# Kernel optimization log

Measured on AMD Instinct MI355X. Metric: run time of the kernel, lower is better.

Reference implementation:

```python
import jax, jax.numpy as jnp
import numpy as np

B, N, DIM, H, DH = 4, 2048, 1024, 16, 64
ROT = 32               # rotary dim (half of head dim)
INNER = H * DH         # 1024


def rotate_every_two(x):
    # (... (d j)) with j=2: pairs (x1, x2) -> (-x2, x1), interleaved back
    x1 = x[..., ::2]
    x2 = x[..., 1::2]
    return jnp.stack((-x2, x1), axis=-1).reshape(x.shape)


def setup_inputs() -> dict:
    key = jax.random.key(0)
    k1, k2, k3 = jax.random.split(key, 3)
    x = jax.random.normal(k1, (B, N, DIM), dtype=jnp.float32)
    # standard rotary sin/cos tables, [N, ROT], pairs share a frequency
    pos = jnp.arange(N, dtype=jnp.float32)[:, None]
    inv_freq = 1.0 / (10000.0 ** (jnp.arange(0, ROT, 2, dtype=jnp.float32) / ROT))
    ang = jnp.repeat(pos * inv_freq, 2, axis=-1)  # [N, ROT]
    sin, cos = jnp.sin(ang), jnp.cos(ang)
    Wqkv = jax.random.normal(k2, (DIM, 3 * INNER), dtype=jnp.float32) * (DIM ** -0.5)
    Wout = jax.random.normal(k3, (INNER, DIM), dtype=jnp.float32) * (INNER ** -0.5)
    return {"x": x, "sin": sin, "cos": cos, "Wqkv": Wqkv, "Wout": Wout}


def reference(x, sin, cos, Wqkv, Wout):
    scale = DH ** -0.5
    qkv = x @ Wqkv                                  # [B, N, 3*INNER]
    q, k, v = jnp.split(qkv, 3, axis=-1)

    def split_heads(t):  # 'b n (h d) -> (b h) n d'
        return t.reshape(B, N, H, DH).transpose(0, 2, 1, 3).reshape(B * H, N, DH)

    q, k, v = map(split_heads, (q, k, v))
    q = q * scale                                   # scale before RoPE (as in source)

    rd = sin.shape[-1]

    def rope(t):
        t_rot, t_pass = t[..., :rd], t[..., rd:]
        t_rot = t_rot * cos + rotate_every_two(t_rot) * sin
        return jnp.concatenate((t_rot, t_pass), axis=-1)

    q, k = rope(q), rope(k)

    sim = jnp.einsum('bid,bjd->bij', q, k)          # [(B*H), N, N]
    attn_w = jax.nn.softmax(sim, axis=-1)
    out = jnp.einsum('bij,bjd->bid', attn_w, v)     # [(B*H), N, DH]

    out = out.reshape(B, H, N, DH).transpose(0, 2, 1, 3).reshape(B, N, INNER)
    return out @ Wout                               # [B, N, DIM]
```

## Files before the change

kernel.cpp:

```cpp
#include <hip/hip_runtime.h>

typedef unsigned short u16;
typedef __attribute__((ext_vector_type(8))) short short8;
typedef __attribute__((ext_vector_type(4))) float f32x4;

#define DEV __device__ __forceinline__

DEV u16 f2bf(float f) {
  unsigned u = __float_as_uint(f);
  u += 0x7FFF + ((u >> 16) & 1);
  return (u16)(u >> 16);
}
DEV float bf2f(u16 b) { return __uint_as_float(((unsigned)b) << 16); }

DEV unsigned pk_trunc(float a, float b) {
  return __builtin_amdgcn_perm(__float_as_uint(b), __float_as_uint(a), 0x07060302u);
}

DEV void g2l16(const u16* g, u16* l) {
  __builtin_amdgcn_global_load_lds((__attribute__((address_space(1))) void*)(g),
                                   (__attribute__((address_space(3))) void*)(l), 16, 0, 0);
}

__global__ __launch_bounds__(256) void k_prep(const float* __restrict__ x,
                                              u16* __restrict__ xb,
                                              const float* __restrict__ Wqkv,
                                              u16* __restrict__ wqkvT,
                                              const float* __restrict__ Wout,
                                              u16* __restrict__ woutT) {
  __shared__ float t[32][33];
  const int blk = blockIdx.x;
  if (blk < 8192) {
    int i = blk * 256 + threadIdx.x;
    float4 v = ((const float4*)x)[i];
    ushort4 r;
    r.x = f2bf(v.x); r.y = f2bf(v.y); r.z = f2bf(v.z); r.w = f2bf(v.w);
    ((ushort4*)xb)[i] = r;
    return;
  }
  const float* W;
  u16* Wt;
  int K = 1024, N, local;
  if (blk < 11264) {
    W = Wqkv; Wt = wqkvT; N = 3072; local = blk - 8192;
  } else {
    W = Wout; Wt = woutT; N = 1024; local = blk - 11264;
  }
  int nb = N / 32;
  int n0 = (local % nb) * 32, k0 = (local / nb) * 32;
  int tx = threadIdx.x & 31, ty = threadIdx.x >> 5;
#pragma unroll
  for (int i = 0; i < 4; ++i)
    t[ty + i * 8][tx] = W[(size_t)(k0 + ty + i * 8) * N + n0 + tx];
  __syncthreads();
#pragma unroll
  for (int i = 0; i < 4; ++i)
    Wt[(size_t)(n0 + ty + i * 8) * K + k0 + tx] = f2bf(t[tx][ty + i * 8]);
}

template <int EPI>
__global__ __launch_bounds__(256) void k_gemm(
    const u16* __restrict__ A, const u16* __restrict__ Bt,
    int M, int N, int K,
    u16* __restrict__ qw, u16* __restrict__ kw, u16* __restrict__ vw,
    float* __restrict__ of, const float* __restrict__ sn,
    const float* __restrict__ cs, float qscale) {
  __shared__ __align__(16) u16 As[128 * 64];
  __shared__ __align__(16) u16 Bs[128 * 64];
  const int t = threadIdx.x;
  const int wv = t >> 6, lane = t & 63;
  const int a15 = lane & 15, g = lane >> 4;
  const int wr = wv >> 1, wc = wv & 1;
  int m0, n0;
  if (EPI == 0) {
    int id = blockIdx.x;
    int c = id & 7, j = id >> 3;
    m0 = (j & 63) * 128;
    n0 = (c * 3 + (j >> 6)) * 128;
  } else {
    m0 = blockIdx.x * 128;
    n0 = blockIdx.y * 128;
  }
  const int gr = lane >> 3, gc = (lane & 7) * 8;

  f32x4 acc[4][4];
#pragma unroll
  for (int i = 0; i < 4; ++i)
#pragma unroll
    for (int j = 0; j < 4; ++j)
#pragma unroll
      for (int r = 0; r < 4; ++r) acc[i][j][r] = 0.f;

  for (int k0 = 0; k0 < K; k0 += 64) {
#pragma unroll
    for (int c4 = 0; c4 < 4; ++c4) {
      int c = wv * 4 + c4;
      g2l16(A + (size_t)(m0 + c * 8 + gr) * K + k0 + gc, &As[c * 512]);
      g2l16(Bt + (size_t)(n0 + c * 8 + gr) * K + k0 + gc, &Bs[c * 512]);
    }
    __syncthreads();
#pragma unroll
    for (int ks = 0; ks < 2; ++ks) {
      short8 af[4], bf[4];
#pragma unroll
      for (int mi = 0; mi < 4; ++mi)
        af[mi] = *(const short8*)&As[(wr * 64 + mi * 16 + a15) * 64 + ks * 32 + g * 8];
#pragma unroll
      for (int ni = 0; ni < 4; ++ni)
        bf[ni] = *(const short8*)&Bs[(wc * 64 + ni * 16 + a15) * 64 + ks * 32 + g * 8];
#pragma unroll
      for (int mi = 0; mi < 4; ++mi)
#pragma unroll
        for (int ni = 0; ni < 4; ++ni)
          acc[mi][ni] = __builtin_amdgcn_mfma_f32_16x16x32_bf16(af[mi], bf[ni], acc[mi][ni], 0, 0, 0);
    }
    __syncthreads();
  }

  if (EPI == 0) {
    const int part = n0 >> 10;
    if (part <= 1) {
      const float sc = (part == 0) ? qscale : 1.f;
      u16* dst = (part == 0) ? qw : kw;
#pragma unroll
      for (int mi = 0; mi < 4; ++mi) {
#pragma unroll
        for (int ni = 0; ni < 4; ++ni) {
          int col = n0 + wc * 64 + ni * 16 + a15;
          int rem = col & 1023, h = rem >> 6, d = rem & 63;
          int row = m0 + wr * 64 + mi * 16 + g * 4;
          int b = row >> 11, n = row & 2047;
          size_t bh = (size_t)b * 16 + h;
#pragma unroll
          for (int r = 0; r < 4; ++r) {
            float v = acc[mi][ni][r];
            float p = __shfl_xor(v, 1);
            float outv = v;
            if (d < 32) {
              int nr = n + r;
              float c = cs[nr * 32 + d], s = sn[nr * 32 + d];
              outv = v * c + ((d & 1) ? p * s : -p * s);
            }
            dst[(bh * 2048 + n + r) * 64 + d] = f2bf(outv * sc);
          }
        }
      }
    } else {
#pragma unroll
      for (int mi = 0; mi < 4; ++mi) {
#pragma unroll
        for (int ni = 0; ni < 4; ++ni) {
          int col = n0 + wc * 64 + ni * 16 + a15;
          int rem = col & 1023, h = rem >> 6, d = rem & 63;
          int row = m0 + wr * 64 + mi * 16 + g * 4;
          int b = row >> 11, n = row & 2047;
          size_t bh = (size_t)b * 16 + h;
          ushort4 pk;
          pk.x = f2bf(acc[mi][ni][0]); pk.y = f2bf(acc[mi][ni][1]);
          pk.z = f2bf(acc[mi][ni][2]); pk.w = f2bf(acc[mi][ni][3]);
          *(ushort4*)&vw[(bh * 64 + d) * 2048 + n] = pk;
        }
      }
    }
  } else {
#pragma unroll
    for (int mi = 0; mi < 4; ++mi)
#pragma unroll
      for (int ni = 0; ni < 4; ++ni) {
        int col = n0 + wc * 64 + ni * 16 + a15;
        int row = m0 + wr * 64 + mi * 16 + g * 4;
#pragma unroll
        for (int r = 0; r < 4; ++r)
          of[(size_t)(row + r) * N + col] = acc[mi][ni][r];
      }
  }
}

__global__ __launch_bounds__(256, 3) void k_attn(
    const u16* __restrict__ q, const u16* __restrict__ kk, const u16* __restrict__ vT,
    u16* __restrict__ o) {
  __shared__ __align__(16) u16 Ks[2][4096];
  __shared__ __align__(16) u16 Vs[2][4096];
  __shared__ __align__(16) u16 Pl[4][1024];
  const int t = threadIdx.x;
  const int w = t >> 6, lane = t & 63;
  const int a15 = lane & 15, g = lane >> 4;
  const int id = blockIdx.x;
  const int bh = (id & 7) | ((id >> 7) << 3);
  const int qb = (id >> 3) & 15;
  const int q0 = qb * 128 + w * 32;
  const size_t hb = (size_t)bh * (2048 * 64);

  short8 qf[2][2];
#pragma unroll
  for (int f = 0; f < 2; ++f)
#pragma unroll
    for (int h = 0; h < 2; ++h)
      qf[f][h] = *(const short8*)&q[hb + (size_t)(q0 + f * 16 + a15) * 64 + h * 32 + g * 8];

  int ksrc[2], vsrc[2];
#pragma unroll
  for (int c = 0; c < 2; ++c) {
    int L = w * 2048 + c * 1024 + lane * 16;
    int row = L >> 7;
    int sb = L ^ ((row & 7) << 4);
    ksrc[c] = sb >> 1;
    vsrc[c] = row * 2048 + ((sb & 127) >> 1);
  }
  const u16* kg = kk + hb;
  const u16* vg = vT + (size_t)bh * (64 * 2048);

#define STAGE(b, j0) do {                                        \
    g2l16(kg + (size_t)(j0) * 64 + ksrc[0], &Ks[b][w * 1024]);   \
    g2l16(kg + (size_t)(j0) * 64 + ksrc[1], &Ks[b][w * 1024 + 512]); \
    g2l16(vg + (j0) + vsrc[0], &Vs[b][w * 1024]);                \
    g2l16(vg + (j0) + vsrc[1], &Vs[b][w * 1024 + 512]);          \
  } while (0)

  const f32x4 z4 = {0.f, 0.f, 0.f, 0.f};
  const short8 ones = {(short)0x3F80, (short)0x3F80, (short)0x3F80, (short)0x3F80,
                       (short)0x3F80, (short)0x3F80, (short)0x3F80, (short)0x3F80};
  f32x4 accO[2][4], ssum[2];
#pragma unroll
  for (int f = 0; f < 2; ++f) {
    ssum[f] = z4;
#pragma unroll
    for (int dc = 0; dc < 4; ++dc) accO[f][dc] = z4;
  }

  STAGE(0, 0);
  int cur = 0;
  for (int jt = 0; jt < 32; ++jt) {
    __syncthreads();
    if (jt < 31) STAGE(cur ^ 1, (jt + 1) * 64);

    f32x4 st[2][4];
    const char* Kb = (const char*)Ks[cur];
    __builtin_amdgcn_s_setprio(1);
#pragma unroll
    for (int jc = 0; jc < 4; ++jc) {
      int row = jc * 16 + a15;
      int sw = (row & 7) << 4;
      short8 ka0 = *(const short8*)(Kb + ((row * 128 + g * 16) ^ sw));
      short8 ka1 = *(const short8*)(Kb + ((row * 128 + 64 + g * 16) ^ sw));
      st[0][jc] = __builtin_amdgcn_mfma_f32_16x16x32_bf16(ka0, qf[0][0], z4, 0, 0, 0);
      st[0][jc] = __builtin_amdgcn_mfma_f32_16x16x32_bf16(ka1, qf[0][1], st[0][jc], 0, 0, 0);
      st[1][jc] = __builtin_amdgcn_mfma_f32_16x16x32_bf16(ka0, qf[1][0], z4, 0, 0, 0);
      st[1][jc] = __builtin_amdgcn_mfma_f32_16x16x32_bf16(ka1, qf[1][1], st[1][jc], 0, 0, 0);
    }
    __builtin_amdgcn_s_setprio(0);
    short8 vf[2][4];
    const char* Vb = (const char*)Vs[cur];
#pragma unroll
    for (int kt = 0; kt < 2; ++kt)
#pragma unroll
      for (int dc = 0; dc < 4; ++dc) {
        int row = dc * 16 + a15;
        vf[kt][dc] = *(const short8*)(Vb + ((row * 128 + kt * 64 + g * 16) ^ ((row & 7) << 4)));
      }
#pragma unroll
    for (int f = 0; f < 2; ++f) {
#pragma unroll
      for (int jc = 0; jc < 4; ++jc) {
        float e0 = __builtin_amdgcn_exp2f(st[f][jc][0]);
        float e1 = __builtin_amdgcn_exp2f(st[f][jc][1]);
        float e2 = __builtin_amdgcn_exp2f(st[f][jc][2]);
        float e3 = __builtin_amdgcn_exp2f(st[f][jc][3]);
        uint2 pw;
        pw.x = pk_trunc(e0, e1);
        pw.y = pk_trunc(e2, e3);
        int byte = (a15 * 128 + (jc * 16 + g * 4) * 2) ^ ((a15 & 7) << 4);
        *(uint2*)((char*)Pl[w] + byte) = pw;
      }
      __builtin_amdgcn_s_setprio(1);
#pragma unroll
      for (int kt = 0; kt < 2; ++kt) {
        int byteA = (a15 * 128 + kt * 64 + g * 16) ^ ((a15 & 7) << 4);
        short8 pa = *(const short8*)((const char*)Pl[w] + byteA);
        ssum[f] = __builtin_amdgcn_mfma_f32_16x16x32_bf16(pa, ones, ssum[f], 0, 0, 0);
#pragma unroll
        for (int dc = 0; dc < 4; ++dc)
          accO[f][dc] = __builtin_amdgcn_mfma_f32_16x16x32_bf16(pa, vf[kt][dc], accO[f][dc], 0, 0, 0);
      }
      __builtin_amdgcn_s_setprio(0);
    }
    cur ^= 1;
  }
#undef STAGE

  const int b = bh >> 4, h = bh & 15;
#pragma unroll
  for (int f = 0; f < 2; ++f) {
    float rs[4];
#pragma unroll
    for (int r = 0; r < 4; ++r) rs[r] = 1.f / ssum[f][r];
#pragma unroll
    for (int dc = 0; dc < 4; ++dc)
#pragma unroll
      for (int r = 0; r < 4; ++r) {
        int n = q0 + f * 16 + g * 4 + r;
        o[((size_t)b * 2048 + n) * 1024 + h * 64 + dc * 16 + a15] = f2bf(accO[f][dc][r] * rs[r]);
      }
  }
}

extern "C" void kernel_launch(void* const* d_in, const int* in_sizes, int n_in,
                              void* d_out, int out_size, void* d_ws, size_t ws_size,
                              hipStream_t stream) {
  const float* x = (const float*)d_in[0];
  const float* sn = (const float*)d_in[1];
  const float* cs = (const float*)d_in[2];
  const float* Wqkv = (const float*)d_in[3];
  const float* Wout = (const float*)d_in[4];
  float* out = (float*)d_out;

  u16* ws = (u16*)d_ws;
  u16* xb = ws;
  u16* wqkvT = xb + 8192ull * 1024;
  u16* woutT = wqkvT + 3072ull * 1024;
  u16* qw = woutT + 1024ull * 1024;
  u16* kw = qw + 64ull * 2048 * 64;
  u16* vw = kw + 64ull * 2048 * 64;
  u16* attn = xb;

  const float qscale = 0.125f * 1.4426950408889634f;

  k_prep<<<12288, 256, 0, stream>>>(x, xb, Wqkv, wqkvT, Wout, woutT);
  k_gemm<0><<<1536, 256, 0, stream>>>(xb, wqkvT, 8192, 3072, 1024,
                                      qw, kw, vw, nullptr, sn, cs, qscale);
  k_attn<<<1024, 256, 0, stream>>>(qw, kw, vw, attn);
  k_gemm<1><<<dim3(64, 8), 256, 0, stream>>>(attn, woutT, 8192, 1024, 1024,
                                             nullptr, nullptr, nullptr, out, nullptr, nullptr, 1.f);
}
```

Before: 216.3 us.

## Replace QKV GEMM with 256x256 double-buffered swizzled 8-wave kernel

The QKV projection moves into a dedicated kernel that uses 256x256 tiles and 8 waves. The global-to-LDS loads are double-buffered and interleaved with MFMA quarter-steps under priority hints and explicit vmcnt waits. An XOR swizzle is applied to the LDS reads to avoid bank conflicts, and the larger tile gives more operand reuse per block. The intent is to hide memory latency and raise MFMA utilisation. In exchange the kernel uses much more LDS and registers and launches only 384 blocks, which may leave the device under-filled. The RoPE, scaling and V-transpose epilogue is unchanged, and the output GEMM template is simplified.

```diff
diff --git a/kernel.cpp b/kernel.cpp
--- a/kernel.cpp
+++ b/kernel.cpp
@@ -58,29 +58,184 @@
     Wt[(size_t)(n0 + ty + i * 8) * K + k0 + tx] = f2bf(t[tx][ty + i * 8]);
 }
 
+__global__ __launch_bounds__(512, 2) void k_gemm0(
+    const u16* __restrict__ A, const u16* __restrict__ Bt,
+    u16* __restrict__ qw, u16* __restrict__ kw, u16* __restrict__ vw,
+    const float* __restrict__ sn, const float* __restrict__ cs, float qscale) {
+  __shared__ __align__(16) u16 As[2][2][8192];
+  __shared__ __align__(16) u16 Bs[2][2][8192];
+  const int tid = threadIdx.x;
+  const int wid = tid >> 6, lane = tid & 63;
+  const int a15 = lane & 15, g = lane >> 4;
+  const int wr = wid >> 2, wc = wid & 3;
+  const int m0 = (blockIdx.x & 31) * 256, n0 = (blockIdx.x >> 5) * 256;
+  const int K = 1024;
+  const int srow = wid * 8 + (lane >> 3);
+  const int scol = ((lane & 7) ^ (lane >> 3)) << 3;
+  const int swz = (a15 & 7) << 4;
+
+#define SA(s, h, l, u) g2l16(A + (size_t)(m0 + (h)*128 + (l)*64 + srow) * K + (u)*64 + scol, \
+                             &As[s][h][(l)*4096 + wid * 512])
+#define SB(s, h, l, u) g2l16(Bt + (size_t)(n0 + (h)*128 + (l)*64 + srow) * K + (u)*64 + scol, \
+                             &Bs[s][h][(l)*4096 + wid * 512])
+
+  f32x4 acc[8][4];
+#pragma unroll
+  for (int i = 0; i < 8; ++i)
+#pragma unroll
+    for (int j = 0; j < 4; ++j)
+#pragma unroll
+      for (int r = 0; r < 4; ++r) acc[i][j][r] = 0.f;
+
+  SA(0,0,0,0); SA(0,1,0,0); SA(0,0,1,0); SA(0,1,1,0);
+  SB(0,0,0,0); SB(0,0,1,0); SB(0,1,0,0); SB(0,1,1,0);
+  SA(1,0,0,1); SA(1,1,0,1); SA(1,0,1,1); SA(1,1,1,1);
+  SB(1,0,0,1); SB(1,0,1,1); SB(1,1,0,1); SB(1,1,1,1);
+  asm volatile("s_waitcnt vmcnt(8)" ::: "memory");
+  __builtin_amdgcn_s_barrier();
+
+  short8 af[4][2], bf[4][2];
+  const int brb = (wc & 1) * 64;
+
+  for (int t = 0; t < 16; ++t) {
+    const int s = t & 1, u = t + 2;
+    const bool st = (u < 16);
+    const char* Ab = (const char*)&As[s][wr][0];
+    const char* Bb = (const char*)&Bs[s][wc >> 1][0];
+#pragma unroll
+    for (int mi = 0; mi < 4; ++mi)
+#pragma unroll
+      for (int ks = 0; ks < 2; ++ks)
+        af[mi][ks] = *(const short8*)(Ab + (((mi * 16 + a15) * 128 + ks * 64 + g * 16) ^ swz));
+#pragma unroll
+    for (int ni = 0; ni < 2; ++ni)
+#pragma unroll
+      for (int ks = 0; ks < 2; ++ks)
+        bf[ni][ks] = *(const short8*)(Bb + (((brb + ni * 16 + a15) * 128 + ks * 64 + g * 16) ^ swz));
+    __builtin_amdgcn_s_barrier();
+    __builtin_amdgcn_s_setprio(1);
+#pragma unroll
+    for (int mi = 0; mi < 4; ++mi)
+#pragma unroll
+      for (int ni = 0; ni < 2; ++ni)
+#pragma unroll
+        for (int ks = 0; ks < 2; ++ks)
+          acc[mi][ni] = __builtin_amdgcn_mfma_f32_16x16x32_bf16(af[mi][ks], bf[ni][ks], acc[mi][ni], 0, 0, 0);
+    __builtin_amdgcn_s_setprio(0);
+    __builtin_amdgcn_s_barrier();
+    if (st) { SA(s, 0, 0, u); SA(s, 1, 0, u); }
+#pragma unroll
+    for (int ni = 0; ni < 2; ++ni)
+#pragma unroll
+      for (int ks = 0; ks < 2; ++ks)
+        bf[2 + ni][ks] = *(const short8*)(Bb + (((brb + (2 + ni) * 16 + a15) * 128 + ks * 64 + g * 16) ^ swz));
+    __builtin_amdgcn_s_barrier();
+    __builtin_amdgcn_s_setprio(1);
+#pragma unroll
+    for (int mi = 0; mi < 4; ++mi)
+#pragma unroll
+      for (int ni = 0; ni < 2; ++ni)
+#pragma unroll
+        for (int ks = 0; ks < 2; ++ks)
+          acc[mi][2 + ni] = __builtin_amdgcn_mfma_f32_16x16x32_bf16(af[mi][ks], bf[2 + ni][ks], acc[mi][2 + ni], 0, 0, 0);
+    __builtin_amdgcn_s_setprio(0);
+    __builtin_amdgcn_s_barrier();
+    if (st) { SB(s, 0, 0, u); SB(s, 0, 1, u); }
+#pragma unroll
+    for (int mi = 0; mi < 4; ++mi)
+#pragma unroll
+      for (int ks = 0; ks < 2; ++ks)
+        af[mi][ks] = *(const short8*)(Ab + ((((64 + mi * 16) + a15) * 128 + ks * 64 + g * 16) ^ swz));
+    __builtin_amdgcn_s_barrier();
+    __builtin_amdgcn_s_setprio(1);
+#pragma unroll
+    for (int mi = 0; mi < 4; ++mi)
+#pragma unroll
+      for (int ni = 0; ni < 2; ++ni)
+#pragma unroll
+        for (int ks = 0; ks < 2; ++ks)
+          acc[4 + mi][ni] = __builtin_amdgcn_mfma_f32_16x16x32_bf16(af[mi][ks], bf[ni][ks], acc[4 + mi][ni], 0, 0, 0);
+    __builtin_amdgcn_s_setprio(0);
+    __builtin_amdgcn_s_barrier();
+    if (st) { SA(s, 0, 1, u); SA(s, 1, 1, u); }
+    __builtin_amdgcn_s_barrier();
+    __builtin_amdgcn_s_setprio(1);
+#pragma unroll
+    for (int mi = 0; mi < 4; ++mi)
+#pragma unroll
+      for (int ni = 0; ni < 2; ++ni)
+#pragma unroll
+        for (int ks = 0; ks < 2; ++ks)
+          acc[4 + mi][2 + ni] = __builtin_amdgcn_mfma_f32_16x16x32_bf16(af[mi][ks], bf[2 + ni][ks], acc[4 + mi][2 + ni], 0, 0, 0);
+    __builtin_amdgcn_s_setprio(0);
+    if (st) { SB(s, 1, 0, u); SB(s, 1, 1, u); }
+    if (t < 14) {
+      asm volatile("s_waitcnt vmcnt(8)" ::: "memory");
+    } else if (t == 14) {
+      asm volatile("s_waitcnt vmcnt(0)" ::: "memory");
+    }
+    __builtin_amdgcn_s_barrier();
+  }
+#undef SA
+#undef SB
+
+  const int part = n0 >> 10;
+  if (part <= 1) {
+    const float sc = (part == 0) ? qscale : 1.f;
+    u16* dst = (part == 0) ? qw : kw;
+#pragma unroll
+    for (int mi = 0; mi < 8; ++mi) {
+#pragma unroll
+      for (int ni = 0; ni < 4; ++ni) {
+        int col = n0 + wc * 64 + ni * 16 + a15;
+        int rem = col & 1023, h = rem >> 6, d = rem & 63;
+        int row = m0 + wr * 128 + mi * 16 + g * 4;
+        int b = row >> 11, n = row & 2047;
+        size_t bh = (size_t)b * 16 + h;
+#pragma unroll
+        for (int r = 0; r < 4; ++r) {
+          float v = acc[mi][ni][r];
+          float p = __shfl_xor(v, 1);
+          float outv = v;
+          if (d < 32) {
+            int nr = n + r;
+            float c = cs[nr * 32 + d], s2 = sn[nr * 32 + d];
+            outv = v * c + ((d & 1) ? p * s2 : -p * s2);
+          }
+          dst[(bh * 2048 + n + r) * 64 + d] = f2bf(outv * sc);
+        }
+      }
+    }
+  } else {
+#pragma unroll
+    for (int mi = 0; mi < 8; ++mi) {
+#pragma unroll
+      for (int ni = 0; ni < 4; ++ni) {
+        int col = n0 + wc * 64 + ni * 16 + a15;
+        int rem = col & 1023, h = rem >> 6, d = rem & 63;
+        int row = m0 + wr * 128 + mi * 16 + g * 4;
+        int b = row >> 11, n = row & 2047;
+        size_t bh = (size_t)b * 16 + h;
+        ushort4 pk;
+        pk.x = f2bf(acc[mi][ni][0]); pk.y = f2bf(acc[mi][ni][1]);
+        pk.z = f2bf(acc[mi][ni][2]); pk.w = f2bf(acc[mi][ni][3]);
+        *(ushort4*)&vw[(bh * 64 + d) * 2048 + n] = pk;
+      }
+    }
+  }
+}
+
 template <int EPI>
 __global__ __launch_bounds__(256) void k_gemm(
     const u16* __restrict__ A, const u16* __restrict__ Bt,
-    int M, int N, int K,
-    u16* __restrict__ qw, u16* __restrict__ kw, u16* __restrict__ vw,
-    float* __restrict__ of, const float* __restrict__ sn,
-    const float* __restrict__ cs, float qscale) {
+    int M, int N, int K, float* __restrict__ of) {
   __shared__ __align__(16) u16 As[128 * 64];
   __shared__ __align__(16) u16 Bs[128 * 64];
   const int t = threadIdx.x;
   const int wv = t >> 6, lane = t & 63;
   const int a15 = lane & 15, g = lane >> 4;
   const int wr = wv >> 1, wc = wv & 1;
-  int m0, n0;
-  if (EPI == 0) {
-    int id = blockIdx.x;
-    int c = id & 7, j = id >> 3;
-    m0 = (j & 63) * 128;
-    n0 = (c * 3 + (j >> 6)) * 128;
-  } else {
-    m0 = blockIdx.x * 128;
-    n0 = blockIdx.y * 128;
-  }
+  const int m0 = blockIdx.x * 128, n0 = blockIdx.y * 128;
   const int gr = lane >> 3, gc = (lane & 7) * 8;
 
   f32x4 acc[4][4];
@@ -117,63 +272,16 @@
     __syncthreads();
   }
 
-  if (EPI == 0) {
-    const int part = n0 >> 10;
-    if (part <= 1) {
-      const float sc = (part == 0) ? qscale : 1.f;
-      u16* dst = (part == 0) ? qw : kw;
-#pragma unroll
-      for (int mi = 0; mi < 4; ++mi) {
-#pragma unroll
-        for (int ni = 0; ni < 4; ++ni) {
-          int col = n0 + wc * 64 + ni * 16 + a15;
-          int rem = col & 1023, h = rem >> 6, d = rem & 63;
-          int row = m0 + wr * 64 + mi * 16 + g * 4;
-          int b = row >> 11, n = row & 2047;
-          size_t bh = (size_t)b * 16 + h;
-#pragma unroll
-          for (int r = 0; r < 4; ++r) {
-            float v = acc[mi][ni][r];
-            float p = __shfl_xor(v, 1);
-            float outv = v;
-            if (d < 32) {
-              int nr = n + r;
-              float c = cs[nr * 32 + d], s = sn[nr * 32 + d];
-              outv = v * c + ((d & 1) ? p * s : -p * s);
-            }
-            dst[(bh * 2048 + n + r) * 64 + d] = f2bf(outv * sc);
-          }
-        }
-      }
-    } else {
-#pragma unroll
-      for (int mi = 0; mi < 4; ++mi) {
-#pragma unroll
-        for (int ni = 0; ni < 4; ++ni) {
-          int col = n0 + wc * 64 + ni * 16 + a15;
-          int rem = col & 1023, h = rem >> 6, d = rem & 63;
-          int row = m0 + wr * 64 + mi * 16 + g * 4;
-          int b = row >> 11, n = row & 2047;
-          size_t bh = (size_t)b * 16 + h;
-          ushort4 pk;
-          pk.x = f2bf(acc[mi][ni][0]); pk.y = f2bf(acc[mi][ni][1]);
-          pk.z = f2bf(acc[mi][ni][2]); pk.w = f2bf(acc[mi][ni][3]);
-          *(ushort4*)&vw[(bh * 64 + d) * 2048 + n] = pk;
-        }
-      }
-    }
-  } else {
-#pragma unroll
-    for (int mi = 0; mi < 4; ++mi)
-#pragma unroll
-      for (int ni = 0; ni < 4; ++ni) {
-        int col = n0 + wc * 64 + ni * 16 + a15;
-        int row = m0 + wr * 64 + mi * 16 + g * 4;
-#pragma unroll
-        for (int r = 0; r < 4; ++r)
-          of[(size_t)(row + r) * N + col] = acc[mi][ni][r];
-      }
-  }
+#pragma unroll
+  for (int mi = 0; mi < 4; ++mi)
+#pragma unroll
+    for (int ni = 0; ni < 4; ++ni) {
+      int col = n0 + wc * 64 + ni * 16 + a15;
+      int row = m0 + wr * 64 + mi * 16 + g * 4;
+#pragma unroll
+      for (int r = 0; r < 4; ++r)
+        of[(size_t)(row + r) * N + col] = acc[mi][ni][r];
+    }
 }
 
 __global__ __launch_bounds__(256, 3) void k_attn(
@@ -326,9 +434,7 @@
   const float qscale = 0.125f * 1.4426950408889634f;
 
   k_prep<<<12288, 256, 0, stream>>>(x, xb, Wqkv, wqkvT, Wout, woutT);
-  k_gemm<0><<<1536, 256, 0, stream>>>(xb, wqkvT, 8192, 3072, 1024,
-                                      qw, kw, vw, nullptr, sn, cs, qscale);
+  k_gemm0<<<384, 512, 0, stream>>>(xb, wqkvT, qw, kw, vw, sn, cs, qscale);
   k_attn<<<1024, 256, 0, stream>>>(qw, kw, vw, attn);
-  k_gemm<1><<<dim3(64, 8), 256, 0, stream>>>(attn, woutT, 8192, 1024, 1024,
-                                             nullptr, nullptr, nullptr, out, nullptr, nullptr, 1.f);
-}
+  k_gemm<1><<<dim3(64, 8), 256, 0, stream>>>(attn, woutT, 8192, 1024, 1024, out);
+}
```

Result: no change. 213.5 us, median of 3 (-1.3%).
